# Kernel tuning notes

Measured on AMD Instinct MI355X. Metric: run time of the kernel, lower is better.

The kernel has to match this reference:

```python
import jax, jax.numpy as jnp
import numpy as np

# dims: batch, seq, d_model, heads, d_ff, experts, top-k, vocab, layers
B, S, D, H, F, E, K, V, L = 2, 1024, 768, 12, 3072, 8, 2, 32000, 2
EPS = 1e-6


def setup_inputs() -> dict:
    key = jax.random.key(0)
    ks = jax.random.split(key, 12)
    n = lambda k, shape: jax.random.normal(k, shape, jnp.float32) * 0.02
    return {
        "tokens": jax.random.randint(ks[0], (B, S), 0, V),
        "emb": n(ks[1], (V, D)),            # token embedding, tied lm_head
        "pos_emb": n(ks[2], (S, D)),        # learned positions (use_rope=False)
        "wq": n(ks[3], (L, D, D)), "bq": jnp.zeros((L, D), jnp.float32),
        "wk": n(ks[4], (L, D, D)), "bk": jnp.zeros((L, D), jnp.float32),
        "wv": n(ks[5], (L, D, D)), "bv": jnp.zeros((L, D), jnp.float32),
        "wo": n(ks[6], (L, D, D)), "bo": jnp.zeros((L, D), jnp.float32),
        "ln1": jnp.ones((L, D), jnp.float32),
        "ln2": jnp.ones((L, D), jnp.float32),
        "gate_w": n(ks[7], (L, D, E)), "gate_b": jnp.zeros((L, E), jnp.float32),
        "w1": n(ks[8], (L, E, D, F)), "b1": jnp.zeros((L, E, F), jnp.float32),
        "w2": n(ks[9], (L, E, F, D)), "b2": jnp.zeros((L, E, D), jnp.float32),
        "ln_f": jnp.ones((D,), jnp.float32),
    }


def rmsnorm(x, w):
    return x * jax.lax.rsqrt(jnp.mean(x * x, axis=-1, keepdims=True) + EPS) * w


def attention(h, wq, bq, wk, bk, wv, bv, wo, bo):
    hd = D // H
    q = (h @ wq + bq).reshape(B, S, H, hd)
    k = (h @ wk + bk).reshape(B, S, H, hd)
    v = (h @ wv + bv).reshape(B, S, H, hd)
    scores = jnp.einsum('bqhd,bkhd->bhqk', q, k) / np.float32(np.sqrt(hd))
    causal = jnp.tril(jnp.ones((S, S), bool))  # mask = tril(ones(S,S))
    scores = jnp.where(causal, scores, jnp.float32(-1e9))
    probs = jax.nn.softmax(scores, axis=-1)
    out = jnp.einsum('bhqk,bkhd->bqhd', probs, v).reshape(B, S, D)
    return out @ wo + bo


def moe(h, gw, gb, w1, b1, w2, b2):
    # router: top-k over gate logits, softmax over the k selected logits
    logits = h @ gw + gb                                   # [B,S,E]
    top_vals, top_idx = jax.lax.top_k(logits, K)           # [B,S,K]
    w = jax.nn.softmax(top_vals, axis=-1)
    # combined per-expert weight = sum over capacity slots of mask*weight
    one_hot = jax.nn.one_hot(top_idx, E, dtype=h.dtype)    # [B,S,K,E]
    cw = jnp.einsum('bsk,bske->bse', w, one_hot)           # [B,S,E]
    # original computes EVERY expert's FFN on the full token batch, masks after
    h1 = jax.nn.gelu(jnp.einsum('bsd,edf->bsef', h, w1) + b1, approximate=False)
    eo = jnp.einsum('bsef,efd->bsed', h1, w2) + b2         # [B,S,E,D]
    return jnp.einsum('bsed,bse->bsd', eo, cw)


def reference(tokens, emb, pos_emb, wq, bq, wk, bk, wv, bv, wo, bo,
              ln1, ln2, gate_w, gate_b, w1, b1, w2, b2, ln_f):
    x = emb[tokens] + pos_emb[None, :S]                    # [B,S,D]
    for l in range(L):
        x = x + attention(rmsnorm(x, ln1[l]), wq[l], bq[l], wk[l], bk[l],
                          wv[l], bv[l], wo[l], bo[l])
        x = x + moe(rmsnorm(x, ln2[l]), gate_w[l], gate_b[l],
                    w1[l], b1[l], w2[l], b2[l])
    x = rmsnorm(x, ln_f)
    return x @ emb.T                                       # tied lm_head -> [B,S,V]
```

## Files before the change

kernel.cpp:

```cpp
#include <hip/hip_runtime.h>
#include <math.h>

#define TT 2048
#define BB 2
#define SS 1024
#define DD 768
#define HH 12
#define FF 3072
#define EE 8
#define VV 32000
#define NLAYER 2
#define QBLK 8

typedef __attribute__((ext_vector_type(8))) short bf16x8;
typedef __attribute__((ext_vector_type(4))) float f32x4;

static __device__ __forceinline__ unsigned short f2b(float f) {
  unsigned u = __float_as_uint(f);
  unsigned r = (u + 0x7fffu + ((u >> 16) & 1u)) >> 16;
  return (unsigned short)r;
}
static __device__ __forceinline__ unsigned int pk2(float a, float b) {
  return (unsigned int)f2b(a) | ((unsigned int)f2b(b) << 16);
}

__global__ __launch_bounds__(256) void k_embed(const int* __restrict__ tok,
    const float* __restrict__ emb, const float* __restrict__ pos,
    float* __restrict__ x) {
  int t = blockIdx.x;
  int s = t & (SS - 1);
  int tk = tok[t];
  const float* er = emb + (size_t)tk * DD;
  const float* pr = pos + (size_t)s * DD;
  float* xr = x + (size_t)t * DD;
  for (int d = threadIdx.x; d < DD; d += 256)
    xr[d] = er[d] + pr[d];
}

__global__ __launch_bounds__(256) void k_rmsnorm(const float* __restrict__ x,
    const float* __restrict__ w, float* __restrict__ out,
    unsigned short* __restrict__ outb) {
  int t = blockIdx.x;
  const float* xr = x + (size_t)t * DD;
  int tid = threadIdx.x;
  float v0 = xr[tid], v1 = xr[tid + 256], v2 = xr[tid + 512];
  float ss = v0 * v0 + v1 * v1 + v2 * v2;
  for (int off = 32; off > 0; off >>= 1) ss += __shfl_down(ss, off, 64);
  __shared__ float ps[4];
  int wid = tid >> 6, lane = tid & 63;
  if (lane == 0) ps[wid] = ss;
  __syncthreads();
  float r = rsqrtf((ps[0] + ps[1] + ps[2] + ps[3]) * (1.0f / DD) + 1e-6f);
  float* orow = out + (size_t)t * DD;
  unsigned short* brow = outb + (size_t)t * DD;
  float o0 = v0 * r * w[tid], o1 = v1 * r * w[tid + 256], o2 = v2 * r * w[tid + 512];
  orow[tid] = o0; orow[tid + 256] = o1; orow[tid + 512] = o2;
  brow[tid] = f2b(o0); brow[tid + 256] = f2b(o1); brow[tid + 512] = f2b(o2);
}

__global__ __launch_bounds__(256) void k_tcvt(const float* __restrict__ src,
    unsigned short* __restrict__ dst, int R, int C, size_t srcZ, size_t dstZ) {
  src += (size_t)blockIdx.z * srcZ;
  dst += (size_t)blockIdx.z * dstZ;
  __shared__ unsigned short tile[32][40];
  int t = threadIdx.x;
  int r = t >> 3, c4 = (t & 7) * 4;
  int r0 = blockIdx.y * 32, c0 = blockIdx.x * 32;
  float4 v = *(const float4*)(src + (size_t)(r0 + r) * C + c0 + c4);
  tile[r][c4 + 0] = f2b(v.x); tile[r][c4 + 1] = f2b(v.y);
  tile[r][c4 + 2] = f2b(v.z); tile[r][c4 + 3] = f2b(v.w);
  __syncthreads();
  int cc = t >> 3, r4 = (t & 7) * 4;
  ushort4 o;
  o.x = tile[r4 + 0][cc]; o.y = tile[r4 + 1][cc];
  o.z = tile[r4 + 2][cc]; o.w = tile[r4 + 3][cc];
  *(ushort4*)(dst + (size_t)(c0 + cc) * R + r0 + r4) = o;
}

__global__ __launch_bounds__(256) void k_cvt(const float* __restrict__ src,
    unsigned short* __restrict__ dst) {
  size_t i = ((size_t)blockIdx.x * 256 + threadIdx.x) * 8;
  float4 a = *(const float4*)(src + i);
  float4 b = *(const float4*)(src + i + 4);
  ushort4 o0, o1;
  o0.x = f2b(a.x); o0.y = f2b(a.y); o0.z = f2b(a.z); o0.w = f2b(a.w);
  o1.x = f2b(b.x); o1.y = f2b(b.y); o1.z = f2b(b.z); o1.w = f2b(b.w);
  *(ushort4*)(dst + i) = o0;
  *(ushort4*)(dst + i + 4) = o1;
}

template<bool EXPERT>
__global__ __launch_bounds__(256) void k_skf32(
    const float* __restrict__ A, const float* __restrict__ W0,
    const float* __restrict__ W1, const float* __restrict__ W2,
    float* __restrict__ part, int M, int Ntot, int Nthird, int K, int KC,
    int nsplit, int prows,
    const int* __restrict__ counts, const int* __restrict__ bases) {
  int s, base = 0, cnt = M, sel = 0, n0;
  const float* W;
  if (EXPERT) {
    int z = blockIdx.z;
    s = z % nsplit;
    int e = z / nsplit;
    cnt = counts[e]; base = bases[e];
    W = W0 + (size_t)e * K * Nthird;
    n0 = blockIdx.x * 128;
  } else {
    s = blockIdx.z;
    int tpn = Nthird >> 7;
    sel = blockIdx.x / tpn;
    n0 = (blockIdx.x - sel * tpn) * 128;
    W = sel == 0 ? W0 : sel == 1 ? W1 : W2;
  }
  int m0 = blockIdx.y * 128;
  if (EXPERT && m0 >= cnt) return;
  int kbase = s * KC;

  __shared__ float As[16][132];
  __shared__ float Bs[16][132];
  int tid = threadIdx.x;
  int tx = tid & 15, ty = tid >> 4;
  int ra = tid >> 1, ka0 = (tid & 1) * 8;
  int kb = tid >> 4, nb0 = (tid & 15) * 8;
  bool arow_ok = !EXPERT || (m0 + ra < cnt);
  const float* Arow = A + (size_t)(EXPERT ? (base + m0 + (arow_ok ? ra : 0))
                                          : (m0 + ra)) * K + kbase;
  float acc[8][8] = {};

  float4 av0 = make_float4(0.f, 0.f, 0.f, 0.f), av1 = av0, bv0, bv1;
  if (arow_ok) {
    av0 = *(const float4*)(Arow + ka0);
    av1 = *(const float4*)(Arow + ka0 + 4);
  }
  {
    const float* Wrow = W + (size_t)(kbase + kb) * Nthird + n0 + nb0;
    bv0 = *(const float4*)(Wrow);
    bv1 = *(const float4*)(Wrow + 4);
  }

  for (int k0 = 0; k0 < KC; k0 += 16) {
    As[ka0 + 0][ra] = av0.x; As[ka0 + 1][ra] = av0.y;
    As[ka0 + 2][ra] = av0.z; As[ka0 + 3][ra] = av0.w;
    As[ka0 + 4][ra] = av1.x; As[ka0 + 5][ra] = av1.y;
    As[ka0 + 6][ra] = av1.z; As[ka0 + 7][ra] = av1.w;
    *(float4*)&Bs[kb][nb0] = bv0;
    *(float4*)&Bs[kb][nb0 + 4] = bv1;
    __syncthreads();
    float4 nav0 = make_float4(0.f, 0.f, 0.f, 0.f), nav1 = nav0, nbv0 = nav0, nbv1 = nav0;
    if (k0 + 16 < KC) {
      if (arow_ok) {
        nav0 = *(const float4*)(Arow + k0 + 16 + ka0);
        nav1 = *(const float4*)(Arow + k0 + 16 + ka0 + 4);
      }
      const float* Wn = W + (size_t)(kbase + k0 + 16 + kb) * Nthird + n0 + nb0;
      nbv0 = *(const float4*)(Wn);
      nbv1 = *(const float4*)(Wn + 4);
    }
#pragma unroll
    for (int kk = 0; kk < 16; kk++) {
      float4 a0 = *(const float4*)&As[kk][ty * 8];
      float4 a1 = *(const float4*)&As[kk][ty * 8 + 4];
      float4 b0 = *(const float4*)&Bs[kk][tx * 8];
      float4 b1 = *(const float4*)&Bs[kk][tx * 8 + 4];
      float a[8] = {a0.x, a0.y, a0.z, a0.w, a1.x, a1.y, a1.z, a1.w};
      float b[8] = {b0.x, b0.y, b0.z, b0.w, b1.x, b1.y, b1.z, b1.w};
#pragma unroll
      for (int i = 0; i < 8; i++) {
#pragma unroll
        for (int j = 0; j < 8; j++) acc[i][j] = fmaf(a[i], b[j], acc[i][j]);
      }
    }
    __syncthreads();
    av0 = nav0; av1 = nav1; bv0 = nbv0; bv1 = nbv1;
  }
#pragma unroll
  for (int i = 0; i < 8; i++) {
    int m = m0 + ty * 8 + i;
    if (EXPERT && m >= cnt) continue;
    size_t prow = EXPERT ? ((size_t)s * prows + base + m) : ((size_t)s * M + m);
    float* orow = part + prow * Ntot + sel * Nthird;
#pragma unroll
    for (int j = 0; j < 8; j++)
      orow[n0 + tx * 8 + j] = acc[i][j];
  }
}

__global__ __launch_bounds__(256) void k_qkvred(const float* __restrict__ part,
    const float* __restrict__ bq, const float* __restrict__ bk,
    const float* __restrict__ bv, float* __restrict__ qb,
    float* __restrict__ kb, float* __restrict__ vb) {
  int t = blockIdx.x;
  for (int c = threadIdx.x; c < 2304; c += 256) {
    float v = part[(size_t)t * 2304 + c] + part[((size_t)TT + t) * 2304 + c];
    if (c < 768)       qb[(size_t)t * DD + c] = v + bq[c];
    else if (c < 1536) kb[(size_t)t * DD + c - 768] = v + bk[c - 768];
    else               vb[(size_t)t * DD + c - 1536] = v + bv[c - 1536];
  }
}

__global__ __launch_bounds__(256) void k_ored(const float* __restrict__ part,
    const float* __restrict__ bo, float* __restrict__ x) {
  int t = blockIdx.x;
  for (int d = threadIdx.x; d < DD; d += 256) {
    float v = part[(size_t)t * DD + d]
            + part[((size_t)TT + t) * DD + d]
            + part[((size_t)2 * TT + t) * DD + d]
            + part[((size_t)3 * TT + t) * DD + d];
    x[(size_t)t * DD + d] += v + bo[d];
  }
}

__global__ __launch_bounds__(256) void k_e2red(const float* __restrict__ part,
    const int* __restrict__ rows, const int* __restrict__ tidx,
    const float* __restrict__ tw, const float* __restrict__ b2,
    float* __restrict__ x) {
  int t = blockIdx.x;
  int r0 = rows[t * 2], r1 = rows[t * 2 + 1];
  int e0 = tidx[t * 2], e1 = tidx[t * 2 + 1];
  float w0 = tw[t * 2], w1 = tw[t * 2 + 1];
  for (int d = threadIdx.x; d < DD; d += 256) {
    float v0 = part[(size_t)r0 * DD + d]
             + part[((size_t)4096 + r0) * DD + d]
             + part[((size_t)8192 + r0) * DD + d]
             + part[((size_t)12288 + r0) * DD + d] + b2[e0 * DD + d];
    float v1 = part[(size_t)r1 * DD + d]
             + part[((size_t)4096 + r1) * DD + d]
             + part[((size_t)8192 + r1) * DD + d]
             + part[((size_t)12288 + r1) * DD + d] + b2[e1 * DD + d];
    x[(size_t)t * DD + d] += w0 * v0 + w1 * v1;
  }
}

__global__ __launch_bounds__(256) void k_attn(const float* __restrict__ q,
    const float* __restrict__ k, const float* __restrict__ v, float* __restrict__ ao) {
  int b = blockIdx.z, hh = blockIdx.y, q0 = blockIdx.x * QBLK;
  __shared__ float qs[QBLK][64];
  __shared__ float sc[QBLK][SS];
  __shared__ float red[QBLK][8];
  int tid = threadIdx.x;
  const size_t hoff = (size_t)b * SS * DD + (size_t)hh * 64;
  for (int i = tid; i < QBLK * 64; i += 256) {
    int qi = i >> 6, d = i & 63;
    qs[qi][d] = q[hoff + (size_t)(q0 + qi) * DD + d];
  }
  __syncthreads();
  int kmax = q0 + QBLK;
  for (int j = tid; j < kmax; j += 256) {
    const float* kr = k + hoff + (size_t)j * DD;
    float p[QBLK];
#pragma unroll
    for (int qi = 0; qi < QBLK; qi++) p[qi] = 0.f;
#pragma unroll 4
    for (int c = 0; c < 16; c++) {
      float4 kv = *(const float4*)(kr + c * 4);
#pragma unroll
      for (int qi = 0; qi < QBLK; qi++)
        p[qi] += qs[qi][c * 4] * kv.x + qs[qi][c * 4 + 1] * kv.y +
                 qs[qi][c * 4 + 2] * kv.z + qs[qi][c * 4 + 3] * kv.w;
    }
#pragma unroll
    for (int qi = 0; qi < QBLK; qi++)
      sc[qi][j] = (j <= q0 + qi) ? p[qi] * 0.125f : -1e30f;
  }
  __syncthreads();
  int wid = tid >> 6, lane = tid & 63;
#pragma unroll
  for (int qi = 0; qi < QBLK; qi++) {
    float mx = -1e30f;
    for (int j = tid; j < kmax; j += 256) mx = fmaxf(mx, sc[qi][j]);
    for (int off = 32; off > 0; off >>= 1) mx = fmaxf(mx, __shfl_down(mx, off, 64));
    if (lane == 0) red[qi][wid] = mx;
  }
  __syncthreads();
#pragma unroll
  for (int qi = 0; qi < QBLK; qi++) {
    float mx = fmaxf(fmaxf(red[qi][0], red[qi][1]), fmaxf(red[qi][2], red[qi][3]));
    float s = 0.f;
    for (int j = tid; j < kmax; j += 256) {
      float e = __expf(sc[qi][j] - mx);
      sc[qi][j] = e;
      s += e;
    }
    for (int off = 32; off > 0; off >>= 1) s += __shfl_down(s, off, 64);
    if (lane == 0) red[qi][4 + wid] = s;
  }
  __syncthreads();
  int d = tid & 63, g = tid >> 6;
  for (int qi = g; qi < QBLK; qi += 4) {
    float inv = 1.f / (red[qi][4] + red[qi][5] + red[qi][6] + red[qi][7]);
    int jend = q0 + qi + 1;
    const float* vp = v + hoff + d;
    float a0 = 0.f, a1 = 0.f, a2 = 0.f, a3 = 0.f;
    int j = 0;
    for (; j + 4 <= jend; j += 4) {
      a0 = fmaf(sc[qi][j],     vp[(size_t)j * DD], a0);
      a1 = fmaf(sc[qi][j + 1], vp[(size_t)(j + 1) * DD], a1);
      a2 = fmaf(sc[qi][j + 2], vp[(size_t)(j + 2) * DD], a2);
      a3 = fmaf(sc[qi][j + 3], vp[(size_t)(j + 3) * DD], a3);
    }
    for (; j < jend; j++) a0 = fmaf(sc[qi][j], vp[(size_t)j * DD], a0);
    float acc = (a0 + a2) + (a1 + a3);
    ao[hoff + (size_t)(q0 + qi) * DD + d] = acc * inv;
  }
}

__global__ __launch_bounds__(256) void k_gate(const float* __restrict__ h,
    const float* __restrict__ gw, const float* __restrict__ gb,
    float* __restrict__ glog) {
  __shared__ float hr[DD];
  int t = blockIdx.x;
  for (int d = threadIdx.x; d < DD; d += 256) hr[d] = h[(size_t)t * DD + d];
  __syncthreads();
  int e = threadIdx.x >> 5, j = threadIdx.x & 31;
  float s = 0.f;
  for (int d = j; d < DD; d += 32) s += hr[d] * gw[d * EE + e];
  for (int off = 16; off > 0; off >>= 1) s += __shfl_down(s, off, 32);
  if (j == 0) glog[t * EE + e] = s + gb[e];
}

__global__ void k_zero(int* counts, int* cursor) {
  int i = threadIdx.x;
  if (i < EE) { counts[i] = 0; cursor[i] = 0; }
}

__global__ void k_router(const float* __restrict__ glog, int* __restrict__ tidx,
    float* __restrict__ tw, int* __restrict__ counts) {
  int t = blockIdx.x * 256 + threadIdx.x;
  if (t >= TT) return;
  float l[EE];
#pragma unroll
  for (int e = 0; e < EE; e++) l[e] = glog[t * EE + e];
  int i0 = 0; float v0 = l[0];
#pragma unroll
  for (int e = 1; e < EE; e++) if (l[e] > v0) { v0 = l[e]; i0 = e; }
  int i1 = -1; float v1 = -1e30f;
#pragma unroll
  for (int e = 0; e < EE; e++) if (e != i0 && l[e] > v1) { v1 = l[e]; i1 = e; }
  float e1 = __expf(v1 - v0);
  float inv = 1.f / (1.f + e1);
  tw[t * 2] = inv; tw[t * 2 + 1] = e1 * inv;
  tidx[t * 2] = i0; tidx[t * 2 + 1] = i1;
  atomicAdd(&counts[i0], 1);
  atomicAdd(&counts[i1], 1);
}

__global__ void k_scan(const int* __restrict__ counts, int* __restrict__ bases,
                       int* __restrict__ cursor) {
  int b = 0;
  for (int e = 0; e < EE; e++) { bases[e] = b; cursor[e] = b; b += counts[e]; }
}

__global__ void k_assign(const int* __restrict__ tidx, int* __restrict__ cursor,
                         int* __restrict__ rows, int* __restrict__ gtok) {
  int t = blockIdx.x * 256 + threadIdx.x;
  if (t >= TT) return;
#pragma unroll
  for (int kk = 0; kk < 2; kk++) {
    int e = tidx[t * 2 + kk];
    int r = atomicAdd(&cursor[e], 1);
    rows[t * 2 + kk] = r;
    gtok[r] = t;
  }
}

__global__ __launch_bounds__(256) void k_expert1(const float* __restrict__ h,
    const float* __restrict__ w1, const float* __restrict__ b1,
    const int* __restrict__ gtok, const int* __restrict__ counts,
    const int* __restrict__ bases, float* __restrict__ gh1) {
  int e = blockIdx.z;
  int cnt = counts[e];
  int m0 = blockIdx.y * 128;
  if (m0 >= cnt) return;
  int base = bases[e];
  int n0 = blockIdx.x * 128;
  const float* W = w1 + (size_t)e * DD * FF;
  __shared__ float As[16][132];
  __shared__ float Bs[16][132];
  int tid = threadIdx.x;
  int tx = tid & 15, ty = tid >> 4;
  int ra = tid >> 1, ka0 = (tid & 1) * 8;
  int kb = tid >> 4, nb0 = (tid & 15) * 8;
  int tok = (m0 + ra < cnt) ? gtok[base + m0 + ra] : -1;
  const float* Arow = h + (size_t)(tok < 0 ? 0 : tok) * DD;
  float acc[8][8] = {};

  float4 av0 = make_float4(0.f, 0.f, 0.f, 0.f), av1 = av0, bv0, bv1;
  if (tok >= 0) {
    av0 = *(const float4*)(Arow + ka0);
    av1 = *(const float4*)(Arow + ka0 + 4);
  }
  {
    const float* Wrow = W + (size_t)kb * FF + n0 + nb0;
    bv0 = *(const float4*)(Wrow);
    bv1 = *(const float4*)(Wrow + 4);
  }

  for (int k0 = 0; k0 < DD; k0 += 16) {
    As[ka0 + 0][ra] = av0.x; As[ka0 + 1][ra] = av0.y;
    As[ka0 + 2][ra] = av0.z; As[ka0 + 3][ra] = av0.w;
    As[ka0 + 4][ra] = av1.x; As[ka0 + 5][ra] = av1.y;
    As[ka0 + 6][ra] = av1.z; As[ka0 + 7][ra] = av1.w;
    *(float4*)&Bs[kb][nb0] = bv0;
    *(float4*)&Bs[kb][nb0 + 4] = bv1;
    __syncthreads();
    float4 nav0 = make_float4(0.f, 0.f, 0.f, 0.f), nav1 = nav0, nbv0 = nav0, nbv1 = nav0;
    if (k0 + 16 < DD) {
      if (tok >= 0) {
        nav0 = *(const float4*)(Arow + k0 + 16 + ka0);
        nav1 = *(const float4*)(Arow + k0 + 16 + ka0 + 4);
      }
      const float* Wn = W + (size_t)(k0 + 16 + kb) * FF + n0 + nb0;
      nbv0 = *(const float4*)(Wn);
      nbv1 = *(const float4*)(Wn + 4);
    }
#pragma unroll
    for (int kk = 0; kk < 16; kk++) {
      float4 a0 = *(const float4*)&As[kk][ty * 8];
      float4 a1 = *(const float4*)&As[kk][ty * 8 + 4];
      float4 b0 = *(const float4*)&Bs[kk][tx * 8];
      float4 b1 = *(const float4*)&Bs[kk][tx * 8 + 4];
      float a[8] = {a0.x, a0.y, a0.z, a0.w, a1.x, a1.y, a1.z, a1.w};
      float b[8] = {b0.x, b0.y, b0.z, b0.w, b1.x, b1.y, b1.z, b1.w};
#pragma unroll
      for (int i = 0; i < 8; i++) {
#pragma unroll
        for (int j = 0; j < 8; j++) acc[i][j] = fmaf(a[i], b[j], acc[i][j]);
      }
    }
    __syncthreads();
    av0 = nav0; av1 = nav1; bv0 = nbv0; bv1 = nbv1;
  }
#pragma unroll
  for (int i = 0; i < 8; i++) {
    int m = m0 + ty * 8 + i;
    if (m >= cnt) continue;
    float* orow = gh1 + (size_t)(base + m) * FF;
#pragma unroll
    for (int j = 0; j < 8; j++) {
      int n = n0 + tx * 8 + j;
      float vv = acc[i][j] + b1[e * FF + n];
      orow[n] = 0.5f * vv * (1.f + erff(vv * 0.70710678118654752f));
    }
  }
}

template<bool EXPERT, bool GATHER, bool BIAS, int EPI, bool BF32>
__global__ __launch_bounds__(256) void k_mfma(
    const unsigned short* __restrict__ A, const void* __restrict__ Bt,
    const float* __restrict__ bias, void* __restrict__ Cv,
    int M, int N, int K,
    const int* __restrict__ gtok, const int* __restrict__ counts,
    const int* __restrict__ bases) {
  int cnt = M, base = 0;
  if (EXPERT) {
    int e = blockIdx.z;
    cnt = counts[e]; base = bases[e];
    if (BIAS) bias += (size_t)e * N;
  }
  int m0 = blockIdx.y * 128;
  if (EXPERT && m0 >= cnt) return;
  int n0 = blockIdx.x * 128;

  __shared__ unsigned short As[128 * 40];
  __shared__ unsigned short Bs[128 * 40];

  int tid = threadIdx.x;
  int srow = tid >> 1;
  int scol = (tid & 1) * 16;

  bool avalid = true;
  const unsigned short* arow;
  if (GATHER) {
    avalid = (m0 + srow) < cnt;
    int tk = avalid ? gtok[base + m0 + srow] : 0;
    arow = A + (size_t)tk * K + scol;
  } else if (EXPERT) {
    avalid = (m0 + srow) < cnt;
    arow = A + (size_t)(base + m0 + (avalid ? srow : 0)) * K + scol;
  } else {
    arow = A + (size_t)(m0 + srow) * K + scol;
  }

  const unsigned short* brow16 = nullptr;
  const float* browf = nullptr;
  if (BF32) {
    browf = (const float*)Bt + (size_t)(n0 + srow) * K + scol;
  } else {
    const unsigned short* B16 = (const unsigned short*)Bt;
    if (EXPERT) B16 += (size_t)blockIdx.z * N * K;
    brow16 = B16 + (size_t)(n0 + srow) * K + scol;
  }

  unsigned short* As_w = As + srow * 40 + scol;
  unsigned short* Bs_w = Bs + srow * 40 + scol;

  int lane = tid & 63, wid = tid >> 6;
  int wr = wid >> 1, wc = wid & 1;
  int l15 = lane & 15, lg = lane >> 4;
  const unsigned short* Ar = As + ((wr * 64 + l15) * 40 + lg * 8);
  const unsigned short* Br = Bs + ((wc * 64 + l15) * 40 + lg * 8);

  f32x4 acc[4][4];
#pragma unroll
  for (int i = 0; i < 4; i++)
#pragma unroll
    for (int j = 0; j < 4; j++) acc[i][j] = (f32x4){0.f, 0.f, 0.f, 0.f};

  for (int k0 = 0; k0 < K; k0 += 32) {
    uint4 av0 = {0, 0, 0, 0}, av1 = {0, 0, 0, 0};
    if (avalid) {
      av0 = *(const uint4*)(arow + k0);
      av1 = *(const uint4*)(arow + k0 + 8);
    }
    uint4 bv0, bv1;
    if (BF32) {
      float4 f0 = *(const float4*)(browf + k0);
      float4 f1 = *(const float4*)(browf + k0 + 4);
      float4 f2 = *(const float4*)(browf + k0 + 8);
      float4 f3 = *(const float4*)(browf + k0 + 12);
      bv0 = make_uint4(pk2(f0.x, f0.y), pk2(f0.z, f0.w), pk2(f1.x, f1.y), pk2(f1.z, f1.w));
      bv1 = make_uint4(pk2(f2.x, f2.y), pk2(f2.z, f2.w), pk2(f3.x, f3.y), pk2(f3.z, f3.w));
    } else {
      bv0 = *(const uint4*)(brow16 + k0);
      bv1 = *(const uint4*)(brow16 + k0 + 8);
    }
    *(uint4*)As_w = av0; *(uint4*)(As_w + 8) = av1;
    *(uint4*)Bs_w = bv0; *(uint4*)(Bs_w + 8) = bv1;
    __syncthreads();
    bf16x8 af[4], bfr[4];
#pragma unroll
    for (int f = 0; f < 4; f++) {
      af[f]  = *(const bf16x8*)(Ar + f * 640);
      bfr[f] = *(const bf16x8*)(Br + f * 640);
    }
#pragma unroll
    for (int i = 0; i < 4; i++)
#pragma unroll
      for (int j = 0; j < 4; j++)
        acc[i][j] = __builtin_amdgcn_mfma_f32_16x16x32_bf16(af[i], bfr[j], acc[i][j], 0, 0, 0);
    __syncthreads();
  }

#pragma unroll
  for (int j = 0; j < 4; j++) {
    int n = n0 + wc * 64 + j * 16 + l15;
    float bb = BIAS ? bias[n] : 0.f;
#pragma unroll
    for (int i = 0; i < 4; i++) {
      int mb = m0 + wr * 64 + i * 16 + lg * 4;
#pragma unroll
      for (int r = 0; r < 4; r++) {
        int m = mb + r;
        if (EXPERT && m >= cnt) continue;
        size_t off = (size_t)(base + m) * N + n;
        float v = acc[i][j][r] + bb;
        if (EPI == 0) {
          ((float*)Cv)[off] = v;
        } else {
          float g = 0.5f * v * (1.f + erff(v * 0.70710678118654752f));
          ((unsigned short*)Cv)[off] = f2b(g);
        }
      }
    }
  }
}

__global__ __launch_bounds__(256) void k_scatter(const float* __restrict__ go,
    const int* __restrict__ rows, const float* __restrict__ tw, float* __restrict__ x) {
  int t = blockIdx.x;
  int r0 = rows[t * 2], r1 = rows[t * 2 + 1];
  float w0 = tw[t * 2], w1 = tw[t * 2 + 1];
  float* xr = x + (size_t)t * DD;
  const float* g0 = go + (size_t)r0 * DD;
  const float* g1 = go + (size_t)r1 * DD;
  for (int d = threadIdx.x; d < DD; d += 256)
    xr[d] += w0 * g0[d] + w1 * g1[d];
}

extern "C" void kernel_launch(void* const* d_in, const int* in_sizes, int n_in,
                              void* d_out, int out_size, void* d_ws, size_t ws_size,
                              hipStream_t stream) {
  (void)in_sizes; (void)n_in; (void)out_size;
  const int* tok   = (const int*)d_in[0];
  const float* emb = (const float*)d_in[1];
  const float* pos = (const float*)d_in[2];
  const float* wq  = (const float*)d_in[3];
  const float* bq  = (const float*)d_in[4];
  const float* wk  = (const float*)d_in[5];
  const float* bk  = (const float*)d_in[6];
  const float* wv  = (const float*)d_in[7];
  const float* bvv = (const float*)d_in[8];
  const float* wo  = (const float*)d_in[9];
  const float* bo  = (const float*)d_in[10];
  const float* ln1 = (const float*)d_in[11];
  const float* ln2 = (const float*)d_in[12];
  const float* gw  = (const float*)d_in[13];
  const float* gb  = (const float*)d_in[14];
  const float* w1  = (const float*)d_in[15];
  const float* b1  = (const float*)d_in[16];
  const float* w2  = (const float*)d_in[17];
  const float* b2  = (const float*)d_in[18];
  const float* lnf = (const float*)d_in[19];

  float* fp = (float*)d_out;
  float* qb   = fp; fp += (size_t)TT * DD;
  float* kb   = fp; fp += (size_t)TT * DD;
  float* vb   = fp; fp += (size_t)TT * DD;
  float* ao   = fp; fp += (size_t)TT * DD;
  float* x    = fp; fp += (size_t)TT * DD;
  float* h    = fp; fp += (size_t)TT * DD;
  float* gh1  = fp; fp += (size_t)TT * 2 * FF;
  float* go   = fp; fp += (size_t)TT * 2 * DD;
  float* glog = fp; fp += (size_t)TT * EE;
  float* tw   = fp; fp += (size_t)TT * 2;
  int* tidx   = (int*)fp; fp += TT * 2;
  int* rows   = (int*)fp; fp += TT * 2;
  int* gtok   = (int*)fp; fp += TT * 2;
  int* counts = (int*)fp; fp += 16;
  int* cursor = (int*)fp; fp += 16;
  int* bases  = (int*)fp; fp += 16;
  unsigned short* hb   = (unsigned short*)fp; fp += (size_t)TT * DD / 2;
  unsigned short* gh1b = (unsigned short*)fp; fp += (size_t)TT * 2 * FF / 2;
  unsigned short* w1t  = (unsigned short*)fp; fp += (size_t)EE * DD * FF / 2;
  unsigned short* w2t  = (unsigned short*)fp; fp += (size_t)EE * FF * DD / 2;
  float* part = fp; fp += (size_t)4 * 4096 * DD;

  unsigned short* hf = (unsigned short*)d_ws;
  unsigned short* embT = (unsigned short*)d_ws + (size_t)TT * DD;
  bool useEmbT = ws_size >= (size_t)TT * DD * 2 + (size_t)VV * DD * 2;

  k_embed<<<TT, 256, 0, stream>>>(tok, emb, pos, x);
  k_tcvt<<<dim3(96, 24, EE), 256, 0, stream>>>(w1 + (size_t)1 * EE * DD * FF, w1t,
      DD, FF, (size_t)DD * FF, (size_t)DD * FF);
  k_tcvt<<<dim3(24, 96, EE), 256, 0, stream>>>(w2 + (size_t)1 * EE * FF * DD, w2t,
      FF, DD, (size_t)FF * DD, (size_t)FF * DD);
  if (useEmbT)
    k_cvt<<<(VV * DD) / (256 * 8), 256, 0, stream>>>(emb, embT);

  for (int l = 0; l < NLAYER; l++) {
    const float* wq_l = wq + (size_t)l * DD * DD;
    const float* wk_l = wk + (size_t)l * DD * DD;
    const float* wv_l = wv + (size_t)l * DD * DD;
    const float* wo_l = wo + (size_t)l * DD * DD;

    k_rmsnorm<<<TT, 256, 0, stream>>>(x, ln1 + (size_t)l * DD, h, hb);
    k_skf32<false><<<dim3(18, 16, 2), 256, 0, stream>>>(h, wq_l, wk_l, wv_l,
        part, TT, 2304, 768, 768, 384, 2, TT, nullptr, nullptr);
    k_qkvred<<<TT, 256, 0, stream>>>(part, bq + (size_t)l * DD, bk + (size_t)l * DD,
        bvv + (size_t)l * DD, qb, kb, vb);
    k_attn<<<dim3(SS / QBLK, HH, BB), 256, 0, stream>>>(qb, kb, vb, ao);
    k_skf32<false><<<dim3(6, 16, 4), 256, 0, stream>>>(ao, wo_l, wo_l, wo_l,
        part, TT, 768, 768, 768, 192, 4, TT, nullptr, nullptr);
    k_ored<<<TT, 256, 0, stream>>>(part, bo + (size_t)l * DD, x);

    k_rmsnorm<<<TT, 256, 0, stream>>>(x, ln2 + (size_t)l * DD, h, hb);
    k_gate<<<TT, 256, 0, stream>>>(h, gw + (size_t)l * DD * EE, gb + (size_t)l * EE, glog);
    k_zero<<<1, 64, 0, stream>>>(counts, cursor);
    k_router<<<TT / 256, 256, 0, stream>>>(glog, tidx, tw, counts);
    k_scan<<<1, 1, 0, stream>>>(counts, bases, cursor);
    k_assign<<<TT / 256, 256, 0, stream>>>(tidx, cursor, rows, gtok);
    if (l < NLAYER - 1) {
      k_expert1<<<dim3(FF / 128, TT / 128, EE), 256, 0, stream>>>(
          h, w1 + (size_t)l * EE * DD * FF, b1 + (size_t)l * EE * FF,
          gtok, counts, bases, gh1);
      k_skf32<true><<<dim3(6, 16, 32), 256, 0, stream>>>(gh1,
          w2 + (size_t)l * EE * FF * DD, nullptr, nullptr,
          part, TT, 768, 768, FF, 768, 4, 4096, counts, bases);
      k_e2red<<<TT, 256, 0, stream>>>(part, rows, tidx, tw,
          b2 + (size_t)l * EE * DD, x);
    } else {
      k_mfma<true, true, true, 2, false><<<dim3(FF / 128, TT / 128, EE), 256, 0, stream>>>(
          hb, w1t, b1 + (size_t)l * EE * FF, gh1b,
          TT, FF, DD, gtok, counts, bases);
      k_mfma<true, false, true, 0, false><<<dim3(DD / 128, TT / 128, EE), 256, 0, stream>>>(
          gh1b, w2t, b2 + (size_t)l * EE * DD, go,
          TT, DD, FF, gtok, counts, bases);
      k_scatter<<<TT, 256, 0, stream>>>(go, rows, tw, x);
    }
  }

  k_rmsnorm<<<TT, 256, 0, stream>>>(x, lnf, h, hf);
  if (useEmbT) {
    k_mfma<false, false, false, 0, false><<<dim3(VV / 128, TT / 128), 256, 0, stream>>>(
        hf, embT, nullptr, (float*)d_out,
        TT, VV, DD, nullptr, nullptr, nullptr);
  } else {
    k_mfma<false, false, false, 0, true><<<dim3(VV / 128, TT / 128), 256, 0, stream>>>(
        hf, emb, nullptr, (float*)d_out,
        TT, VV, DD, nullptr, nullptr, nullptr);
  }
}
```

Baseline: 2.283 ms.

## Use direct global-to-LDS loads in bf16 MFMA GEMM and retile fp32 expert GEMMs

The bf16 MFMA GEMM now fills its shared-memory tiles with global_load_lds 16-byte transfers instead of staging through registers, and drops the row padding to fit that layout. The fp32 weight-conversion path moves into a separate kernel. The layer-0 fp32 expert GEMMs get new 64x256 tiles with 128 threads and a padded B layout. Removing the padding may add LDS bank conflicts, and the new fp32 kernels lose the register prefetch double-buffering.

```diff
diff --git a/kernel.cpp b/kernel.cpp
--- a/kernel.cpp
+++ b/kernel.cpp
@@ -14,6 +14,10 @@
 
 typedef __attribute__((ext_vector_type(8))) short bf16x8;
 typedef __attribute__((ext_vector_type(4))) float f32x4;
+
+#define GL16(ldst, gsrc) __builtin_amdgcn_global_load_lds( \
+    (const __attribute__((address_space(1))) void*)(gsrc), \
+    (__attribute__((address_space(3))) void*)(ldst), 16, 0, 0)
 
 static __device__ __forceinline__ unsigned short f2b(float f) {
   unsigned u = __float_as_uint(f);
@@ -89,31 +93,17 @@
   *(ushort4*)(dst + i + 4) = o1;
 }
 
-template<bool EXPERT>
 __global__ __launch_bounds__(256) void k_skf32(
     const float* __restrict__ A, const float* __restrict__ W0,
     const float* __restrict__ W1, const float* __restrict__ W2,
     float* __restrict__ part, int M, int Ntot, int Nthird, int K, int KC,
-    int nsplit, int prows,
-    const int* __restrict__ counts, const int* __restrict__ bases) {
-  int s, base = 0, cnt = M, sel = 0, n0;
-  const float* W;
-  if (EXPERT) {
-    int z = blockIdx.z;
-    s = z % nsplit;
-    int e = z / nsplit;
-    cnt = counts[e]; base = bases[e];
-    W = W0 + (size_t)e * K * Nthird;
-    n0 = blockIdx.x * 128;
-  } else {
-    s = blockIdx.z;
-    int tpn = Nthird >> 7;
-    sel = blockIdx.x / tpn;
-    n0 = (blockIdx.x - sel * tpn) * 128;
-    W = sel == 0 ? W0 : sel == 1 ? W1 : W2;
-  }
+    int nsplit, int prows) {
+  int s = blockIdx.z;
+  int tpn = Nthird >> 7;
+  int sel = blockIdx.x / tpn;
+  int n0 = (blockIdx.x - sel * tpn) * 128;
+  const float* W = sel == 0 ? W0 : sel == 1 ? W1 : W2;
   int m0 = blockIdx.y * 128;
-  if (EXPERT && m0 >= cnt) return;
   int kbase = s * KC;
 
   __shared__ float As[16][132];
@@ -122,16 +112,12 @@
   int tx = tid & 15, ty = tid >> 4;
   int ra = tid >> 1, ka0 = (tid & 1) * 8;
   int kb = tid >> 4, nb0 = (tid & 15) * 8;
-  bool arow_ok = !EXPERT || (m0 + ra < cnt);
-  const float* Arow = A + (size_t)(EXPERT ? (base + m0 + (arow_ok ? ra : 0))
-                                          : (m0 + ra)) * K + kbase;
+  const float* Arow = A + (size_t)(m0 + ra) * K + kbase;
   float acc[8][8] = {};
 
-  float4 av0 = make_float4(0.f, 0.f, 0.f, 0.f), av1 = av0, bv0, bv1;
-  if (arow_ok) {
-    av0 = *(const float4*)(Arow + ka0);
-    av1 = *(const float4*)(Arow + ka0 + 4);
-  }
+  float4 av0 = *(const float4*)(Arow + ka0);
+  float4 av1 = *(const float4*)(Arow + ka0 + 4);
+  float4 bv0, bv1;
   {
     const float* Wrow = W + (size_t)(kbase + kb) * Nthird + n0 + nb0;
     bv0 = *(const float4*)(Wrow);
@@ -148,10 +134,8 @@
     __syncthreads();
     float4 nav0 = make_float4(0.f, 0.f, 0.f, 0.f), nav1 = nav0, nbv0 = nav0, nbv1 = nav0;
     if (k0 + 16 < KC) {
-      if (arow_ok) {
-        nav0 = *(const float4*)(Arow + k0 + 16 + ka0);
-        nav1 = *(const float4*)(Arow + k0 + 16 + ka0 + 4);
-      }
+      nav0 = *(const float4*)(Arow + k0 + 16 + ka0);
+      nav1 = *(const float4*)(Arow + k0 + 16 + ka0 + 4);
       const float* Wn = W + (size_t)(kbase + k0 + 16 + kb) * Nthird + n0 + nb0;
       nbv0 = *(const float4*)(Wn);
       nbv1 = *(const float4*)(Wn + 4);
@@ -176,12 +160,163 @@
 #pragma unroll
   for (int i = 0; i < 8; i++) {
     int m = m0 + ty * 8 + i;
-    if (EXPERT && m >= cnt) continue;
-    size_t prow = EXPERT ? ((size_t)s * prows + base + m) : ((size_t)s * M + m);
+    size_t prow = (size_t)s * M + m;
     float* orow = part + prow * Ntot + sel * Nthird;
 #pragma unroll
     for (int j = 0; j < 8; j++)
       orow[n0 + tx * 8 + j] = acc[i][j];
+  }
+}
+
+__global__ __launch_bounds__(128) void k_e1w(const float* __restrict__ h,
+    const float* __restrict__ w1, const float* __restrict__ b1,
+    const int* __restrict__ gtok, const int* __restrict__ counts,
+    const int* __restrict__ bases, float* __restrict__ gh1) {
+  int e = blockIdx.z;
+  int cnt = counts[e];
+  int m0 = blockIdx.y * 64;
+  if (m0 >= cnt) return;
+  int base = bases[e];
+  int n0 = blockIdx.x * 256;
+  const float* W = w1 + (size_t)e * DD * FF;
+  __shared__ float As[16][68];
+  __shared__ float Bs[16][272];
+  int tid = threadIdx.x;
+  int tx = tid & 15, ty = tid >> 4;
+  int ra = tid >> 1, ka0 = (tid & 1) * 8;
+  int kb = tid >> 3, nb0 = (tid & 7) * 32;
+  int g0 = (tid & 7) * 2;
+  float* bw0 = &Bs[kb][g0 * 17];
+  float* bw1 = &Bs[kb][(g0 + 1) * 17];
+  int tok = (m0 + ra < cnt) ? gtok[base + m0 + ra] : -1;
+  const float* Arow = h + (size_t)(tok < 0 ? 0 : tok) * DD;
+  float acc[8][16] = {};
+  for (int k0 = 0; k0 < DD; k0 += 16) {
+    float4 av0 = make_float4(0.f, 0.f, 0.f, 0.f), av1 = av0;
+    if (tok >= 0) {
+      av0 = *(const float4*)(Arow + k0 + ka0);
+      av1 = *(const float4*)(Arow + k0 + ka0 + 4);
+    }
+    As[ka0 + 0][ra] = av0.x; As[ka0 + 1][ra] = av0.y;
+    As[ka0 + 2][ra] = av0.z; As[ka0 + 3][ra] = av0.w;
+    As[ka0 + 4][ra] = av1.x; As[ka0 + 5][ra] = av1.y;
+    As[ka0 + 6][ra] = av1.z; As[ka0 + 7][ra] = av1.w;
+    const float* Wr = W + (size_t)(k0 + kb) * FF + n0 + nb0;
+    *(float4*)(bw0 + 0)  = *(const float4*)(Wr + 0);
+    *(float4*)(bw0 + 4)  = *(const float4*)(Wr + 4);
+    *(float4*)(bw0 + 8)  = *(const float4*)(Wr + 8);
+    *(float4*)(bw0 + 12) = *(const float4*)(Wr + 12);
+    *(float4*)(bw1 + 0)  = *(const float4*)(Wr + 16);
+    *(float4*)(bw1 + 4)  = *(const float4*)(Wr + 20);
+    *(float4*)(bw1 + 8)  = *(const float4*)(Wr + 24);
+    *(float4*)(bw1 + 12) = *(const float4*)(Wr + 28);
+    __syncthreads();
+#pragma unroll
+    for (int kk = 0; kk < 16; kk++) {
+      float4 a0 = *(const float4*)&As[kk][ty * 8];
+      float4 a1 = *(const float4*)&As[kk][ty * 8 + 4];
+      const float* bp = &Bs[kk][tx * 17];
+      float4 b0 = *(const float4*)(bp);
+      float4 b1 = *(const float4*)(bp + 4);
+      float4 b2 = *(const float4*)(bp + 8);
+      float4 b3 = *(const float4*)(bp + 12);
+      float a[8] = {a0.x, a0.y, a0.z, a0.w, a1.x, a1.y, a1.z, a1.w};
+      float b[16] = {b0.x, b0.y, b0.z, b0.w, b1.x, b1.y, b1.z, b1.w,
+                     b2.x, b2.y, b2.z, b2.w, b3.x, b3.y, b3.z, b3.w};
+#pragma unroll
+      for (int i = 0; i < 8; i++) {
+#pragma unroll
+        for (int j = 0; j < 16; j++) acc[i][j] = fmaf(a[i], b[j], acc[i][j]);
+      }
+    }
+    __syncthreads();
+  }
+#pragma unroll
+  for (int i = 0; i < 8; i++) {
+    int m = m0 + ty * 8 + i;
+    if (m >= cnt) continue;
+    float* orow = gh1 + (size_t)(base + m) * FF;
+#pragma unroll
+    for (int j = 0; j < 16; j++) {
+      int n = n0 + tx * 16 + j;
+      float vv = acc[i][j] + b1[e * FF + n];
+      orow[n] = 0.5f * vv * (1.f + erff(vv * 0.70710678118654752f));
+    }
+  }
+}
+
+__global__ __launch_bounds__(128) void k_e2w(const float* __restrict__ gh1,
+    const float* __restrict__ w2, const int* __restrict__ counts,
+    const int* __restrict__ bases, float* __restrict__ part) {
+  int z = blockIdx.z;
+  int s = z & 3, e = z >> 2;
+  int cnt = counts[e];
+  int m0 = blockIdx.y * 64;
+  if (m0 >= cnt) return;
+  int base = bases[e];
+  int n0 = blockIdx.x * 256;
+  int kbase = s * 768;
+  const float* W = w2 + (size_t)e * FF * DD;
+  __shared__ float As[16][68];
+  __shared__ float Bs[16][272];
+  int tid = threadIdx.x;
+  int tx = tid & 15, ty = tid >> 4;
+  int ra = tid >> 1, ka0 = (tid & 1) * 8;
+  int kb = tid >> 3, nb0 = (tid & 7) * 32;
+  int g0 = (tid & 7) * 2;
+  float* bw0 = &Bs[kb][g0 * 17];
+  float* bw1 = &Bs[kb][(g0 + 1) * 17];
+  bool arow_ok = (m0 + ra < cnt);
+  const float* Arow = gh1 + (size_t)(base + (arow_ok ? m0 + ra : 0)) * FF + kbase;
+  float acc[8][16] = {};
+  for (int k0 = 0; k0 < 768; k0 += 16) {
+    float4 av0 = make_float4(0.f, 0.f, 0.f, 0.f), av1 = av0;
+    if (arow_ok) {
+      av0 = *(const float4*)(Arow + k0 + ka0);
+      av1 = *(const float4*)(Arow + k0 + ka0 + 4);
+    }
+    As[ka0 + 0][ra] = av0.x; As[ka0 + 1][ra] = av0.y;
+    As[ka0 + 2][ra] = av0.z; As[ka0 + 3][ra] = av0.w;
+    As[ka0 + 4][ra] = av1.x; As[ka0 + 5][ra] = av1.y;
+    As[ka0 + 6][ra] = av1.z; As[ka0 + 7][ra] = av1.w;
+    const float* Wr = W + (size_t)(kbase + k0 + kb) * DD + n0 + nb0;
+    *(float4*)(bw0 + 0)  = *(const float4*)(Wr + 0);
+    *(float4*)(bw0 + 4)  = *(const float4*)(Wr + 4);
+    *(float4*)(bw0 + 8)  = *(const float4*)(Wr + 8);
+    *(float4*)(bw0 + 12) = *(const float4*)(Wr + 12);
+    *(float4*)(bw1 + 0)  = *(const float4*)(Wr + 16);
+    *(float4*)(bw1 + 4)  = *(const float4*)(Wr + 20);
+    *(float4*)(bw1 + 8)  = *(const float4*)(Wr + 24);
+    *(float4*)(bw1 + 12) = *(const float4*)(Wr + 28);
+    __syncthreads();
+#pragma unroll
+    for (int kk = 0; kk < 16; kk++) {
+      float4 a0 = *(const float4*)&As[kk][ty * 8];
+      float4 a1 = *(const float4*)&As[kk][ty * 8 + 4];
+      const float* bp = &Bs[kk][tx * 17];
+      float4 b0 = *(const float4*)(bp);
+      float4 b1 = *(const float4*)(bp + 4);
+      float4 b2 = *(const float4*)(bp + 8);
+      float4 b3 = *(const float4*)(bp + 12);
+      float a[8] = {a0.x, a0.y, a0.z, a0.w, a1.x, a1.y, a1.z, a1.w};
+      float b[16] = {b0.x, b0.y, b0.z, b0.w, b1.x, b1.y, b1.z, b1.w,
+                     b2.x, b2.y, b2.z, b2.w, b3.x, b3.y, b3.z, b3.w};
+#pragma unroll
+      for (int i = 0; i < 8; i++) {
+#pragma unroll
+        for (int j = 0; j < 16; j++) acc[i][j] = fmaf(a[i], b[j], acc[i][j]);
+      }
+    }
+    __syncthreads();
+  }
+#pragma unroll
+  for (int i = 0; i < 8; i++) {
+    int m = m0 + ty * 8 + i;
+    if (m >= cnt) continue;
+    float* orow = part + ((size_t)s * 4096 + base + m) * DD;
+#pragma unroll
+    for (int j = 0; j < 16; j++)
+      orow[n0 + tx * 16 + j] = acc[i][j];
   }
 }
 
@@ -363,90 +498,9 @@
   }
 }
 
-__global__ __launch_bounds__(256) void k_expert1(const float* __restrict__ h,
-    const float* __restrict__ w1, const float* __restrict__ b1,
-    const int* __restrict__ gtok, const int* __restrict__ counts,
-    const int* __restrict__ bases, float* __restrict__ gh1) {
-  int e = blockIdx.z;
-  int cnt = counts[e];
-  int m0 = blockIdx.y * 128;
-  if (m0 >= cnt) return;
-  int base = bases[e];
-  int n0 = blockIdx.x * 128;
-  const float* W = w1 + (size_t)e * DD * FF;
-  __shared__ float As[16][132];
-  __shared__ float Bs[16][132];
-  int tid = threadIdx.x;
-  int tx = tid & 15, ty = tid >> 4;
-  int ra = tid >> 1, ka0 = (tid & 1) * 8;
-  int kb = tid >> 4, nb0 = (tid & 15) * 8;
-  int tok = (m0 + ra < cnt) ? gtok[base + m0 + ra] : -1;
-  const float* Arow = h + (size_t)(tok < 0 ? 0 : tok) * DD;
-  float acc[8][8] = {};
-
-  float4 av0 = make_float4(0.f, 0.f, 0.f, 0.f), av1 = av0, bv0, bv1;
-  if (tok >= 0) {
-    av0 = *(const float4*)(Arow + ka0);
-    av1 = *(const float4*)(Arow + ka0 + 4);
-  }
-  {
-    const float* Wrow = W + (size_t)kb * FF + n0 + nb0;
-    bv0 = *(const float4*)(Wrow);
-    bv1 = *(const float4*)(Wrow + 4);
-  }
-
-  for (int k0 = 0; k0 < DD; k0 += 16) {
-    As[ka0 + 0][ra] = av0.x; As[ka0 + 1][ra] = av0.y;
-    As[ka0 + 2][ra] = av0.z; As[ka0 + 3][ra] = av0.w;
-    As[ka0 + 4][ra] = av1.x; As[ka0 + 5][ra] = av1.y;
-    As[ka0 + 6][ra] = av1.z; As[ka0 + 7][ra] = av1.w;
-    *(float4*)&Bs[kb][nb0] = bv0;
-    *(float4*)&Bs[kb][nb0 + 4] = bv1;
-    __syncthreads();
-    float4 nav0 = make_float4(0.f, 0.f, 0.f, 0.f), nav1 = nav0, nbv0 = nav0, nbv1 = nav0;
-    if (k0 + 16 < DD) {
-      if (tok >= 0) {
-        nav0 = *(const float4*)(Arow + k0 + 16 + ka0);
-        nav1 = *(const float4*)(Arow + k0 + 16 + ka0 + 4);
-      }
-      const float* Wn = W + (size_t)(k0 + 16 + kb) * FF + n0 + nb0;
-      nbv0 = *(const float4*)(Wn);
-      nbv1 = *(const float4*)(Wn + 4);
-    }
-#pragma unroll
-    for (int kk = 0; kk < 16; kk++) {
-      float4 a0 = *(const float4*)&As[kk][ty * 8];
-      float4 a1 = *(const float4*)&As[kk][ty * 8 + 4];
-      float4 b0 = *(const float4*)&Bs[kk][tx * 8];
-      float4 b1 = *(const float4*)&Bs[kk][tx * 8 + 4];
-      float a[8] = {a0.x, a0.y, a0.z, a0.w, a1.x, a1.y, a1.z, a1.w};
-      float b[8] = {b0.x, b0.y, b0.z, b0.w, b1.x, b1.y, b1.z, b1.w};
-#pragma unroll
-      for (int i = 0; i < 8; i++) {
-#pragma unroll
-        for (int j = 0; j < 8; j++) acc[i][j] = fmaf(a[i], b[j], acc[i][j]);
-      }
-    }
-    __syncthreads();
-    av0 = nav0; av1 = nav1; bv0 = nbv0; bv1 = nbv1;
-  }
-#pragma unroll
-  for (int i = 0; i < 8; i++) {
-    int m = m0 + ty * 8 + i;
-    if (m >= cnt) continue;
-    float* orow = gh1 + (size_t)(base + m) * FF;
-#pragma unroll
-    for (int j = 0; j < 8; j++) {
-      int n = n0 + tx * 8 + j;
-      float vv = acc[i][j] + b1[e * FF + n];
-      orow[n] = 0.5f * vv * (1.f + erff(vv * 0.70710678118654752f));
-    }
-  }
-}
-
-template<bool EXPERT, bool GATHER, bool BIAS, int EPI, bool BF32>
-__global__ __launch_bounds__(256) void k_mfma(
-    const unsigned short* __restrict__ A, const void* __restrict__ Bt,
+template<bool EXPERT, bool GATHER, bool BIAS, int EPI>
+__global__ __launch_bounds__(256) void k_mfma2(
+    const unsigned short* __restrict__ A, const unsigned short* __restrict__ Bt,
     const float* __restrict__ bias, void* __restrict__ Cv,
     int M, int N, int K,
     const int* __restrict__ gtok, const int* __restrict__ counts,
@@ -456,49 +510,47 @@
     int e = blockIdx.z;
     cnt = counts[e]; base = bases[e];
     if (BIAS) bias += (size_t)e * N;
+    Bt += (size_t)e * N * K;
   }
   int m0 = blockIdx.y * 128;
   if (EXPERT && m0 >= cnt) return;
   int n0 = blockIdx.x * 128;
 
-  __shared__ unsigned short As[128 * 40];
-  __shared__ unsigned short Bs[128 * 40];
-
-  int tid = threadIdx.x;
-  int srow = tid >> 1;
-  int scol = (tid & 1) * 16;
-
-  bool avalid = true;
-  const unsigned short* arow;
+  __shared__ unsigned short As[128 * 32];
+  __shared__ unsigned short Bs[128 * 32];
+
+  int tid = threadIdx.x, lane = tid & 63, w = tid >> 6;
+  int r0 = w * 16 + (lane >> 2);
+  int r1 = 64 + r0;
+  int kc = (lane & 3) * 8;
+
+  const unsigned short *pA0, *pA1;
   if (GATHER) {
-    avalid = (m0 + srow) < cnt;
-    int tk = avalid ? gtok[base + m0 + srow] : 0;
-    arow = A + (size_t)tk * K + scol;
+    int t0 = (m0 + r0 < cnt) ? gtok[base + m0 + r0] : 0;
+    int t1 = (m0 + r1 < cnt) ? gtok[base + m0 + r1] : 0;
+    pA0 = A + (size_t)t0 * K + kc;
+    pA1 = A + (size_t)t1 * K + kc;
   } else if (EXPERT) {
-    avalid = (m0 + srow) < cnt;
-    arow = A + (size_t)(base + m0 + (avalid ? srow : 0)) * K + scol;
+    int q0_ = (m0 + r0 < cnt) ? base + m0 + r0 : base;
+    int q1_ = (m0 + r1 < cnt) ? base + m0 + r1 : base;
+    pA0 = A + (size_t)q0_ * K + kc;
+    pA1 = A + (size_t)q1_ * K + kc;
   } else {
-    arow = A + (size_t)(m0 + srow) * K + scol;
-  }
-
-  const unsigned short* brow16 = nullptr;
-  const float* browf = nullptr;
-  if (BF32) {
-    browf = (const float*)Bt + (size_t)(n0 + srow) * K + scol;
-  } else {
-    const unsigned short* B16 = (const unsigned short*)Bt;
-    if (EXPERT) B16 += (size_t)blockIdx.z * N * K;
-    brow16 = B16 + (size_t)(n0 + srow) * K + scol;
-  }
-
-  unsigned short* As_w = As + srow * 40 + scol;
-  unsigned short* Bs_w = Bs + srow * 40 + scol;
-
-  int lane = tid & 63, wid = tid >> 6;
-  int wr = wid >> 1, wc = wid & 1;
+    pA0 = A + (size_t)(m0 + r0) * K + kc;
+    pA1 = A + (size_t)(m0 + r1) * K + kc;
+  }
+  const unsigned short* pB0 = Bt + (size_t)(n0 + r0) * K + kc;
+  const unsigned short* pB1 = Bt + (size_t)(n0 + r1) * K + kc;
+
+  unsigned short* dA0 = As + w * 512;
+  unsigned short* dA1 = As + 2048 + w * 512;
+  unsigned short* dB0 = Bs + w * 512;
+  unsigned short* dB1 = Bs + 2048 + w * 512;
+
+  int wr = w >> 1, wc = w & 1;
   int l15 = lane & 15, lg = lane >> 4;
-  const unsigned short* Ar = As + ((wr * 64 + l15) * 40 + lg * 8);
-  const unsigned short* Br = Bs + ((wc * 64 + l15) * 40 + lg * 8);
+  const unsigned short* Ar = As + ((wr * 64 + l15) * 32 + lg * 8);
+  const unsigned short* Br = Bs + ((wc * 64 + l15) * 32 + lg * 8);
 
   f32x4 acc[4][4];
 #pragma unroll
@@ -507,31 +559,16 @@
     for (int j = 0; j < 4; j++) acc[i][j] = (f32x4){0.f, 0.f, 0.f, 0.f};
 
   for (int k0 = 0; k0 < K; k0 += 32) {
-    uint4 av0 = {0, 0, 0, 0}, av1 = {0, 0, 0, 0};
-    if (avalid) {
-      av0 = *(const uint4*)(arow + k0);
-      av1 = *(const uint4*)(arow + k0 + 8);
-    }
-    uint4 bv0, bv1;
-    if (BF32) {
-      float4 f0 = *(const float4*)(browf + k0);
-      float4 f1 = *(const float4*)(browf + k0 + 4);
-      float4 f2 = *(const float4*)(browf + k0 + 8);
-      float4 f3 = *(const float4*)(browf + k0 + 12);
-      bv0 = make_uint4(pk2(f0.x, f0.y), pk2(f0.z, f0.w), pk2(f1.x, f1.y), pk2(f1.z, f1.w));
-      bv1 = make_uint4(pk2(f2.x, f2.y), pk2(f2.z, f2.w), pk2(f3.x, f3.y), pk2(f3.z, f3.w));
-    } else {
-      bv0 = *(const uint4*)(brow16 + k0);
-      bv1 = *(const uint4*)(brow16 + k0 + 8);
-    }
-    *(uint4*)As_w = av0; *(uint4*)(As_w + 8) = av1;
-    *(uint4*)Bs_w = bv0; *(uint4*)(Bs_w + 8) = bv1;
+    GL16(dA0, pA0 + k0);
+    GL16(dA1, pA1 + k0);
+    GL16(dB0, pB0 + k0);
+    GL16(dB1, pB1 + k0);
     __syncthreads();
     bf16x8 af[4], bfr[4];
 #pragma unroll
     for (int f = 0; f < 4; f++) {
-      af[f]  = *(const bf16x8*)(Ar + f * 640);
-      bfr[f] = *(const bf16x8*)(Br + f * 640);
+      af[f]  = *(const bf16x8*)(Ar + f * 512);
+      bfr[f] = *(const bf16x8*)(Br + f * 512);
     }
 #pragma unroll
     for (int i = 0; i < 4; i++)
@@ -561,6 +598,68 @@
           ((unsigned short*)Cv)[off] = f2b(g);
         }
       }
+    }
+  }
+}
+
+__global__ __launch_bounds__(256) void k_mfma_bf32(
+    const unsigned short* __restrict__ A, const float* __restrict__ Bf,
+    float* __restrict__ C, int M, int N, int K) {
+  int m0 = blockIdx.y * 128;
+  int n0 = blockIdx.x * 128;
+  __shared__ unsigned short As[128 * 40];
+  __shared__ unsigned short Bs[128 * 40];
+  int tid = threadIdx.x;
+  int srow = tid >> 1;
+  int scol = (tid & 1) * 16;
+  const unsigned short* arow = A + (size_t)(m0 + srow) * K + scol;
+  const float* browf = Bf + (size_t)(n0 + srow) * K + scol;
+  unsigned short* As_w = As + srow * 40 + scol;
+  unsigned short* Bs_w = Bs + srow * 40 + scol;
+  int lane = tid & 63, wid = tid >> 6;
+  int wr = wid >> 1, wc = wid & 1;
+  int l15 = lane & 15, lg = lane >> 4;
+  const unsigned short* Ar = As + ((wr * 64 + l15) * 40 + lg * 8);
+  const unsigned short* Br = Bs + ((wc * 64 + l15) * 40 + lg * 8);
+  f32x4 acc[4][4];
+#pragma unroll
+  for (int i = 0; i < 4; i++)
+#pragma unroll
+    for (int j = 0; j < 4; j++) acc[i][j] = (f32x4){0.f, 0.f, 0.f, 0.f};
+  for (int k0 = 0; k0 < K; k0 += 32) {
+    uint4 av0 = *(const uint4*)(arow + k0);
+    uint4 av1 = *(const uint4*)(arow + k0 + 8);
+    float4 f0 = *(const float4*)(browf + k0);
+    float4 f1 = *(const float4*)(browf + k0 + 4);
+    float4 f2 = *(const float4*)(browf + k0 + 8);
+    float4 f3 = *(const float4*)(browf + k0 + 12);
+    uint4 bv0 = make_uint4(pk2(f0.x, f0.y), pk2(f0.z, f0.w), pk2(f1.x, f1.y), pk2(f1.z, f1.w));
+    uint4 bv1 = make_uint4(pk2(f2.x, f2.y), pk2(f2.z, f2.w), pk2(f3.x, f3.y), pk2(f3.z, f3.w));
+    *(uint4*)As_w = av0; *(uint4*)(As_w + 8) = av1;
+    *(uint4*)Bs_w = bv0; *(uint4*)(Bs_w + 8) = bv1;
+    __syncthreads();
+    bf16x8 af[4], bfr[4];
+#pragma unroll
+    for (int f = 0; f < 4; f++) {
+      af[f]  = *(const bf16x8*)(Ar + f * 640);
+      bfr[f] = *(const bf16x8*)(Br + f * 640);
+    }
+#pragma unroll
+    for (int i = 0; i < 4; i++)
+#pragma unroll
+      for (int j = 0; j < 4; j++)
+        acc[i][j] = __builtin_amdgcn_mfma_f32_16x16x32_bf16(af[i], bfr[j], acc[i][j], 0, 0, 0);
+    __syncthreads();
+  }
+#pragma unroll
+  for (int j = 0; j < 4; j++) {
+    int n = n0 + wc * 64 + j * 16 + l15;
+#pragma unroll
+    for (int i = 0; i < 4; i++) {
+      int mb = m0 + wr * 64 + i * 16 + lg * 4;
+#pragma unroll
+      for (int r = 0; r < 4; r++)
+        C[(size_t)(mb + r) * N + n] = acc[i][j][r];
     }
   }
 }
@@ -644,13 +743,13 @@
     const float* wo_l = wo + (size_t)l * DD * DD;
 
     k_rmsnorm<<<TT, 256, 0, stream>>>(x, ln1 + (size_t)l * DD, h, hb);
-    k_skf32<false><<<dim3(18, 16, 2), 256, 0, stream>>>(h, wq_l, wk_l, wv_l,
-        part, TT, 2304, 768, 768, 384, 2, TT, nullptr, nullptr);
+    k_skf32<<<dim3(18, 16, 2), 256, 0, stream>>>(h, wq_l, wk_l, wv_l,
+        part, TT, 2304, 768, 768, 384, 2, TT);
     k_qkvred<<<TT, 256, 0, stream>>>(part, bq + (size_t)l * DD, bk + (size_t)l * DD,
         bvv + (size_t)l * DD, qb, kb, vb);
     k_attn<<<dim3(SS / QBLK, HH, BB), 256, 0, stream>>>(qb, kb, vb, ao);
-    k_skf32<false><<<dim3(6, 16, 4), 256, 0, stream>>>(ao, wo_l, wo_l, wo_l,
-        part, TT, 768, 768, 768, 192, 4, TT, nullptr, nullptr);
+    k_skf32<<<dim3(6, 16, 4), 256, 0, stream>>>(ao, wo_l, wo_l, wo_l,
+        part, TT, 768, 768, 768, 192, 4, TT);
     k_ored<<<TT, 256, 0, stream>>>(part, bo + (size_t)l * DD, x);
 
     k_rmsnorm<<<TT, 256, 0, stream>>>(x, ln2 + (size_t)l * DD, h, hb);
@@ -660,19 +759,18 @@
     k_scan<<<1, 1, 0, stream>>>(counts, bases, cursor);
     k_assign<<<TT / 256, 256, 0, stream>>>(tidx, cursor, rows, gtok);
     if (l < NLAYER - 1) {
-      k_expert1<<<dim3(FF / 128, TT / 128, EE), 256, 0, stream>>>(
+      k_e1w<<<dim3(FF / 256, 32, EE), 128, 0, stream>>>(
           h, w1 + (size_t)l * EE * DD * FF, b1 + (size_t)l * EE * FF,
           gtok, counts, bases, gh1);
-      k_skf32<true><<<dim3(6, 16, 32), 256, 0, stream>>>(gh1,
-          w2 + (size_t)l * EE * FF * DD, nullptr, nullptr,
-          part, TT, 768, 768, FF, 768, 4, 4096, counts, bases);
+      k_e2w<<<dim3(3, 32, 32), 128, 0, stream>>>(
+          gh1, w2 + (size_t)l * EE * FF * DD, counts, bases, part);
       k_e2red<<<TT, 256, 0, stream>>>(part, rows, tidx, tw,
           b2 + (size_t)l * EE * DD, x);
     } else {
-      k_mfma<true, true, true, 2, false><<<dim3(FF / 128, TT / 128, EE), 256, 0, stream>>>(
+      k_mfma2<true, true, true, 2><<<dim3(FF / 128, TT / 128, EE), 256, 0, stream>>>(
           hb, w1t, b1 + (size_t)l * EE * FF, gh1b,
           TT, FF, DD, gtok, counts, bases);
-      k_mfma<true, false, true, 0, false><<<dim3(DD / 128, TT / 128, EE), 256, 0, stream>>>(
+      k_mfma2<true, false, true, 0><<<dim3(DD / 128, TT / 128, EE), 256, 0, stream>>>(
           gh1b, w2t, b2 + (size_t)l * EE * DD, go,
           TT, DD, FF, gtok, counts, bases);
       k_scatter<<<TT, 256, 0, stream>>>(go, rows, tw, x);
@@ -681,12 +779,11 @@
 
   k_rmsnorm<<<TT, 256, 0, stream>>>(x, lnf, h, hf);
   if (useEmbT) {
-    k_mfma<false, false, false, 0, false><<<dim3(VV / 128, TT / 128), 256, 0, stream>>>(
+    k_mfma2<false, false, false, 0><<<dim3(VV / 128, TT / 128), 256, 0, stream>>>(
         hf, embT, nullptr, (float*)d_out,
         TT, VV, DD, nullptr, nullptr, nullptr);
   } else {
-    k_mfma<false, false, false, 0, true><<<dim3(VV / 128, TT / 128), 256, 0, stream>>>(
-        hf, emb, nullptr, (float*)d_out,
-        TT, VV, DD, nullptr, nullptr, nullptr);
-  }
-}
+    k_mfma_bf32<<<dim3(VV / 128, TT / 128), 256, 0, stream>>>(
+        hf, emb, (float*)d_out, TT, VV, DD);
+  }
+}
```

Result: slower. 3.753 ms (+64.3%).
